# Performance work log

Hardware: AMD Instinct MI355X
Metric: run time of the kernel (lower is better)

The kernel has to match this reference:

```python
import jax, jax.numpy as jnp
import numpy as np

EPS = 1e-5

def _conv(x, w, b, groups=1, pad=0):
    # x: NCHW, w: OIHW (I = in_ch/groups)
    y = jax.lax.conv_general_dilated(
        x, w, window_strides=(1, 1), padding=[(pad, pad), (pad, pad)],
        feature_group_count=groups,
        dimension_numbers=('NCHW', 'OIHW', 'NCHW'))
    return y + b[None, :, None, None]

def _bn(x, g, b, m, v):
    scale = g * jax.lax.rsqrt(v + EPS)
    return x * scale[None, :, None, None] + (b - m * scale)[None, :, None, None]

def _block(x, w_dw, b_dw, w_pw, b_pw, g, b, m, v, groups):
    h = _conv(x, w_dw, b_dw, groups=groups, pad=1)   # 3x3 grouped conv
    h = _conv(h, w_pw, b_pw)                          # 1x1 pointwise 2C->C
    return jax.nn.relu(_bn(h, g, b, m, v))

def setup_inputs() -> dict:
    key = jax.random.key(0)
    ks = jax.random.split(key, 16)
    B, C, H, W = 4, 256, 64, 64
    s = 0.02  # small weight scale to keep softmax logits well-conditioned
    return {
        'x1': jax.random.normal(ks[0], (B, C, H, W), jnp.float32),
        'x2': jax.random.normal(ks[1], (B, C, H, W), jnp.float32),
        'w1_dw': jax.random.normal(ks[2], (2 * C, 2, 3, 3), jnp.float32) * s,
        'b1_dw': jnp.zeros((2 * C,), jnp.float32),
        'w1_pw': jax.random.normal(ks[3], (C, 2 * C, 1, 1), jnp.float32) * s,
        'b1_pw': jnp.zeros((C,), jnp.float32),
        'bn1_g': jnp.ones((C,), jnp.float32),
        'bn1_b': jnp.zeros((C,), jnp.float32),
        'bn1_m': jnp.zeros((C,), jnp.float32),
        'bn1_v': jnp.ones((C,), jnp.float32),
        'w2_dw': jax.random.normal(ks[4], (2 * C, 2, 3, 3), jnp.float32) * s,
        'b2_dw': jnp.zeros((2 * C,), jnp.float32),
        'w2_pw': jax.random.normal(ks[5], (C, 2 * C, 1, 1), jnp.float32) * s,
        'b2_pw': jnp.zeros((C,), jnp.float32),
        'bn2_g': jnp.ones((C,), jnp.float32),
        'bn2_b': jnp.zeros((C,), jnp.float32),
        'bn2_m': jnp.zeros((C,), jnp.float32),
        'bn2_v': jnp.ones((C,), jnp.float32),
        'wq': jax.random.normal(ks[6], (C // 8, C, 1, 1), jnp.float32) * s,
        'bq': jnp.zeros((C // 8,), jnp.float32),
        'wk': jax.random.normal(ks[7], (C // 8, C, 1, 1), jnp.float32) * s,
        'bk': jnp.zeros((C // 8,), jnp.float32),
        'wv': jax.random.normal(ks[8], (C, C, 1, 1), jnp.float32) * s,
        'bv': jnp.zeros((C,), jnp.float32),
        'gamma': jnp.ones((1,), jnp.float32),
    }

def reference(x1, x2,
              w1_dw, b1_dw, w1_pw, b1_pw, bn1_g, bn1_b, bn1_m, bn1_v,
              w2_dw, b2_dw, w2_pw, b2_pw, bn2_g, bn2_b, bn2_m, bn2_v,
              wq, bq, wk, bk, wv, bv, gamma):
    B, C, H, W = x1.shape
    N = H * W
    sub = x1 - x2
    concat1 = jnp.concatenate([sub, x1], axis=1)  # [B,2C,H,W]
    concat2 = jnp.concatenate([sub, x2], axis=1)
    x3 = _block(concat1, w1_dw, b1_dw, w1_pw, b1_pw, bn1_g, bn1_b, bn1_m, bn1_v, groups=C)
    x4 = _block(concat2, w2_dw, b2_dw, w2_pw, b2_pw, bn2_g, bn2_b, bn2_m, bn2_v, groups=C)
    q = _conv(x4, wq, bq).reshape(B, -1, N)   # [B, C//8, N]
    k = _conv(x3, wk, bk).reshape(B, -1, N)   # [B, C//8, N]
    v = _conv(x3, wv, bv).reshape(B, C, N)    # [B, C, N]
    energy = jnp.einsum('bdq,bdk->bqk', q, k)          # [B, N, N]
    attn = jax.nn.softmax(energy, axis=-1)
    out = jnp.einsum('bck,bqk->bcq', v, attn)          # [B, C, N]
    out = out.reshape(B, C, H, W)
    return gamma[0] * out + x1
```

## Files before the change

### kernel.cpp

```cpp
#include <hip/hip_runtime.h>
#include <hip/hip_bf16.h>

#define EPSB 1e-5f

typedef __hip_bfloat16 bf16;
typedef __attribute__((ext_vector_type(8))) short bf16x8;
typedef __attribute__((ext_vector_type(4))) float f32x4;

__device__ __forceinline__ unsigned short f2bu(float x) {
  bf16 h = __float2bfloat16(x);
  return *reinterpret_cast<unsigned short*>(&h);
}
__device__ __forceinline__ unsigned int pk2(float lo, float hi) {
  return ((unsigned int)f2bu(hi) << 16) | (unsigned int)f2bu(lo);
}

__global__ __launch_bounds__(256) void k_dwconv3(
    const float* __restrict__ x1, const float* __restrict__ x2,
    const float* __restrict__ w1, const float* __restrict__ b1,
    const float* __restrict__ w2, const float* __restrict__ b2,
    bf16* __restrict__ h1, bf16* __restrict__ h2) {
  __shared__ float img[2 * 64 * 64];
  int g = blockIdx.x, b = blockIdx.y;
  int t = threadIdx.x;
  int row = t >> 2, x0 = (t & 3) * 16;
  size_t obase = (((size_t)(b * 512 + 2 * g)) << 12) + row * 64 + x0;

  auto stencil = [&](const float* wp, float bs0, float bs1, bf16* hout) {
    float o0[16], o1[16];
#pragma unroll
    for (int i = 0; i < 16; i++) { o0[i] = bs0; o1[i] = bs1; }
#pragma unroll
    for (int ch = 0; ch < 2; ch++) {
      float wa[9], wb[9];
#pragma unroll
      for (int i = 0; i < 9; i++) { wa[i] = wp[ch * 9 + i]; wb[i] = wp[18 + ch * 9 + i]; }
      const float* ib = img + ch * 4096;
#pragma unroll
      for (int ky = 0; ky < 3; ky++) {
        int yy = row + ky - 1;
        if (yy < 0 || yy > 63) continue;
        float v[18];
#pragma unroll
        for (int c = 0; c < 18; c++) {
          int xx = x0 + c - 1;
          v[c] = (xx >= 0 && xx < 64) ? ib[yy * 64 + xx] : 0.f;
        }
        float a0 = wa[ky * 3], a1 = wa[ky * 3 + 1], a2 = wa[ky * 3 + 2];
        float c0 = wb[ky * 3], c1 = wb[ky * 3 + 1], c2 = wb[ky * 3 + 2];
#pragma unroll
        for (int i = 0; i < 16; i++) {
          o0[i] += a0 * v[i] + a1 * v[i + 1] + a2 * v[i + 2];
          o1[i] += c0 * v[i] + c1 * v[i + 1] + c2 * v[i + 2];
        }
      }
    }
    uint4 u0 = {pk2(o0[0], o0[1]), pk2(o0[2], o0[3]), pk2(o0[4], o0[5]), pk2(o0[6], o0[7])};
    uint4 u1 = {pk2(o0[8], o0[9]), pk2(o0[10], o0[11]), pk2(o0[12], o0[13]), pk2(o0[14], o0[15])};
    *(uint4*)&hout[obase] = u0;
    *(uint4*)&hout[obase + 8] = u1;
    uint4 w0 = {pk2(o1[0], o1[1]), pk2(o1[2], o1[3]), pk2(o1[4], o1[5]), pk2(o1[6], o1[7])};
    uint4 w1v = {pk2(o1[8], o1[9]), pk2(o1[10], o1[11]), pk2(o1[12], o1[13]), pk2(o1[14], o1[15])};
    *(uint4*)&hout[obase + 4096] = w0;
    *(uint4*)&hout[obase + 4096 + 8] = w1v;
  };

  if (g < 128) {
    const float4* p1 = (const float4*)(x1 + ((size_t)(b * 256 + 2 * g) << 12));
    const float4* p2 = (const float4*)(x2 + ((size_t)(b * 256 + 2 * g) << 12));
#pragma unroll
    for (int u = 0; u < 8; u++) {
      int i = u * 256 + t;
      float4 a = p1[i], c = p2[i];
      float4 d = {a.x - c.x, a.y - c.y, a.z - c.z, a.w - c.w};
      ((float4*)img)[i] = d;
    }
  } else {
    const float4* p1 = (const float4*)(x1 + ((size_t)(b * 256 + 2 * (g - 128)) << 12));
#pragma unroll
    for (int u = 0; u < 8; u++) {
      int i = u * 256 + t;
      ((float4*)img)[i] = p1[i];
    }
  }
  __syncthreads();
  stencil(w1 + (size_t)(2 * g) * 18, b1[2 * g], b1[2 * g + 1], h1);

  if (g >= 128) {
    __syncthreads();
    const float4* p2 = (const float4*)(x2 + ((size_t)(b * 256 + 2 * (g - 128)) << 12));
#pragma unroll
    for (int u = 0; u < 8; u++) {
      int i = u * 256 + t;
      ((float4*)img)[i] = p2[i];
    }
    __syncthreads();
  }
  stencil(w2 + (size_t)(2 * g) * 18, b2[2 * g], b2[2 * g + 1], h2);
}

__global__ __launch_bounds__(256) void k_gemm_mfma(
    const bf16* __restrict__ In, const float* __restrict__ W,
    const float* __restrict__ bias,
    const float* __restrict__ bng, const float* __restrict__ bnb,
    const float* __restrict__ bnm, const float* __restrict__ bnv,
    int has_bn, int relu,
    bf16* __restrict__ Out, int IC) {
  __shared__ __align__(16) bf16 Al[128][40];
  __shared__ __align__(16) bf16 Bl[64][40];

  int t = threadIdx.x;
  int w = t >> 6, lane = t & 63, l16 = lane & 15, quad = lane >> 4;
  int wr = w >> 1, wc = w & 1;
  int p0 = blockIdx.x * 64;
  int oc0 = blockIdx.y * 128;
  int b = blockIdx.z;
  const bf16* Inb = In + (size_t)b * IC * 4096;

  f32x4 acc[4][2];
#pragma unroll
  for (int mi = 0; mi < 4; mi++)
#pragma unroll
    for (int nj = 0; nj < 2; nj++) acc[mi][nj] = (f32x4){0.f, 0.f, 0.f, 0.f};

  int sl = t & 15, srp = t >> 4;
  int ocl = t >> 1, kb = (t & 1) * 16;

  for (int kc = 0; kc < IC; kc += 32) {
    __syncthreads();
    {
      const float* src = W + (size_t)(oc0 + ocl) * IC + kc + kb;
      float4 f0 = *(const float4*)(src);
      float4 f1 = *(const float4*)(src + 4);
      float4 f2 = *(const float4*)(src + 8);
      float4 f3 = *(const float4*)(src + 12);
      uint4 u0 = {pk2(f0.x, f0.y), pk2(f0.z, f0.w), pk2(f1.x, f1.y), pk2(f1.z, f1.w)};
      uint4 u1 = {pk2(f2.x, f2.y), pk2(f2.z, f2.w), pk2(f3.x, f3.y), pk2(f3.z, f3.w)};
      *(uint4*)&Al[ocl][kb] = u0;
      *(uint4*)&Al[ocl][kb + 8] = u1;
    }
    {
      const unsigned short* re = (const unsigned short*)(Inb + (size_t)(kc + 2 * srp) * 4096 + p0 + sl);
#pragma unroll
      for (int j = 0; j < 4; j++) {
        unsigned int e = re[j * 16];
        unsigned int o = re[4096 + j * 16];
        *(unsigned int*)&Bl[j * 16 + sl][2 * srp] = e | (o << 16);
      }
    }
    __syncthreads();
    bf16x8 af[4], bv[2];
#pragma unroll
    for (int mi = 0; mi < 4; mi++)
      af[mi] = *(const bf16x8*)&Al[wr * 64 + mi * 16 + l16][quad * 8];
#pragma unroll
    for (int nj = 0; nj < 2; nj++)
      bv[nj] = *(const bf16x8*)&Bl[wc * 32 + nj * 16 + l16][quad * 8];
#pragma unroll
    for (int mi = 0; mi < 4; mi++)
#pragma unroll
      for (int nj = 0; nj < 2; nj++)
        acc[mi][nj] = __builtin_amdgcn_mfma_f32_16x16x32_bf16(
            af[mi], bv[nj], acc[mi][nj], 0, 0, 0);
  }

#pragma unroll
  for (int mi = 0; mi < 4; mi++) {
    int ocb = oc0 + wr * 64 + mi * 16 + quad * 4;
    float4 bs4 = *(const float4*)&bias[ocb];
    float4 sc4 = {1.f, 1.f, 1.f, 1.f}, sh4 = bs4;
    if (has_bn) {
      float4 g4 = *(const float4*)&bng[ocb];
      float4 b4 = *(const float4*)&bnb[ocb];
      float4 m4 = *(const float4*)&bnm[ocb];
      float4 v4 = *(const float4*)&bnv[ocb];
      sc4.x = g4.x * rsqrtf(v4.x + EPSB); sh4.x = bs4.x * sc4.x + b4.x - m4.x * sc4.x;
      sc4.y = g4.y * rsqrtf(v4.y + EPSB); sh4.y = bs4.y * sc4.y + b4.y - m4.y * sc4.y;
      sc4.z = g4.z * rsqrtf(v4.z + EPSB); sh4.z = bs4.z * sc4.z + b4.z - m4.z * sc4.z;
      sc4.w = g4.w * rsqrtf(v4.w + EPSB); sh4.w = bs4.w * sc4.w + b4.w - m4.w * sc4.w;
    }
    float sc[4] = {sc4.x, sc4.y, sc4.z, sc4.w};
    float sh[4] = {sh4.x, sh4.y, sh4.z, sh4.w};
#pragma unroll
    for (int nj = 0; nj < 2; nj++) {
      int p = p0 + wc * 32 + nj * 16 + l16;
#pragma unroll
      for (int r = 0; r < 4; r++) {
        float val = acc[mi][nj][r] * sc[r] + sh[r];
        if (relu) val = fmaxf(val, 0.f);
        Out[(((size_t)(b * 256 + ocb + r)) << 12) + p] = __float2bfloat16(val);
      }
    }
  }
}

__global__ __launch_bounds__(256) void k_gemm_qk(
    const bf16* __restrict__ x4, const bf16* __restrict__ x3,
    const float* __restrict__ wq, const float* __restrict__ wk,
    const float* __restrict__ bq, const float* __restrict__ bk,
    bf16* __restrict__ qb, bf16* __restrict__ kb) {
  __shared__ __align__(16) bf16 Al[32][40];
  __shared__ __align__(16) bf16 Bl[128][40];

  int t = threadIdx.x;
  int w = t >> 6, lane = t & 63, l16 = lane & 15, quad = lane >> 4;
  int p0 = blockIdx.x * 128;
  int b = blockIdx.z;
  const bf16* In  = (blockIdx.y == 0) ? x4 : x3;
  const float* W  = (blockIdx.y == 0) ? wq : wk;
  const float* bi = (blockIdx.y == 0) ? bq : bk;
  bf16* Out       = (blockIdx.y == 0) ? qb : kb;
  const bf16* Inb = In + (size_t)b * 256 * 4096;

  f32x4 acc[2][2];
#pragma unroll
  for (int mi = 0; mi < 2; mi++)
#pragma unroll
    for (int nj = 0; nj < 2; nj++) acc[mi][nj] = (f32x4){0.f, 0.f, 0.f, 0.f};

  int aocl = t >> 3, akb = (t & 7) * 4;
  int sl = t & 15, srp = t >> 4;

  for (int kc = 0; kc < 256; kc += 32) {
    __syncthreads();
    {
      const float* src = W + (size_t)aocl * 256 + kc + akb;
      float4 f0 = *(const float4*)(src);
      uint2 u = {pk2(f0.x, f0.y), pk2(f0.z, f0.w)};
      *(uint2*)&Al[aocl][akb] = u;
    }
    {
      const unsigned short* re = (const unsigned short*)(Inb + (size_t)(kc + 2 * srp) * 4096 + p0 + sl);
#pragma unroll
      for (int j = 0; j < 8; j++) {
        unsigned int e = re[j * 16];
        unsigned int o = re[4096 + j * 16];
        *(unsigned int*)&Bl[j * 16 + sl][2 * srp] = e | (o << 16);
      }
    }
    __syncthreads();
    bf16x8 af[2], bv[2];
#pragma unroll
    for (int mi = 0; mi < 2; mi++)
      af[mi] = *(const bf16x8*)&Al[mi * 16 + l16][quad * 8];
#pragma unroll
    for (int nj = 0; nj < 2; nj++)
      bv[nj] = *(const bf16x8*)&Bl[w * 32 + nj * 16 + l16][quad * 8];
#pragma unroll
    for (int mi = 0; mi < 2; mi++)
#pragma unroll
      for (int nj = 0; nj < 2; nj++)
        acc[mi][nj] = __builtin_amdgcn_mfma_f32_16x16x32_bf16(
            af[mi], bv[nj], acc[mi][nj], 0, 0, 0);
  }

#pragma unroll
  for (int mi = 0; mi < 2; mi++) {
    int ocb = mi * 16 + quad * 4;
    float4 bs4 = *(const float4*)&bi[ocb];
    float bs[4] = {bs4.x, bs4.y, bs4.z, bs4.w};
#pragma unroll
    for (int nj = 0; nj < 2; nj++) {
      int p = p0 + w * 32 + nj * 16 + l16;
      float v0 = acc[mi][nj][0] + bs[0];
      float v1 = acc[mi][nj][1] + bs[1];
      float v2 = acc[mi][nj][2] + bs[2];
      float v3 = acc[mi][nj][3] + bs[3];
      uint2 u = {pk2(v0, v1), pk2(v2, v3)};
      *(uint2*)&Out[((size_t)(b * 4096) + p) * 32 + ocb] = u;
    }
  }
}

__global__ __launch_bounds__(512, 4) void k_attn_mfma(
    const bf16* __restrict__ qb, const bf16* __restrict__ kb,
    const bf16* __restrict__ vb, const float* __restrict__ x1,
    const float* __restrict__ gamma, float* __restrict__ out) {
  __shared__ __align__(16) bf16 Pl[2][64 * 128];
  __shared__ float lsumw[8][64];

  int t = threadIdx.x;
  int w = t >> 6, lane = t & 63;
  int l16 = lane & 15, quad = lane >> 4;
  int bx = blockIdx.x;
  int q0 = (bx >> 1) * 64;
  int chalf = bx & 1;
  int b = blockIdx.y;

  const bf16* kbb = kb + (size_t)b * 4096 * 32;
  const bf16* vbb = vb + ((size_t)(b * 256 + chalf * 128)) * 4096;

  bf16x8 qf[4];
#pragma unroll
  for (int nj = 0; nj < 4; nj++)
    qf[nj] = *(const bf16x8*)(qb + ((size_t)(b * 4096 + q0 + nj * 16 + l16)) * 32 + quad * 8);

  f32x4 acc[4];
#pragma unroll
  for (int nj = 0; nj < 4; nj++) acc[nj] = (f32x4){0.f, 0.f, 0.f, 0.f};
  float lpart[4] = {0.f, 0.f, 0.f, 0.f};

  const bf16* kptr = kbb + ((size_t)(w * 16 + l16)) * 32 + quad * 8;
  const bf16* vptr = vbb + ((size_t)(w * 16 + l16)) * 4096 + quad * 8;

  int c16w = w * 2 + (quad >> 1);
  int off8 = (quad & 1) * 4;

  auto load_kv = [&](int j0, bf16x8& kf, bf16x8 vf[4]) {
    kf = *(const bf16x8*)(kptr + (size_t)j0 * 32);
#pragma unroll
    for (int kc = 0; kc < 4; kc++)
      vf[kc] = *(const bf16x8*)(vptr + j0 + kc * 32);
  };

  auto s_phase = [&](const bf16x8& kf, int pb) {
    bf16* P = Pl[pb];
#pragma unroll
    for (int nj = 0; nj < 4; nj++) {
      f32x4 s = __builtin_amdgcn_mfma_f32_16x16x32_bf16(
          kf, qf[nj], (f32x4){0.f, 0.f, 0.f, 0.f}, 0, 0, 0);
      float p0f = __expf(fminf(s[0], 80.f));
      float p1f = __expf(fminf(s[1], 80.f));
      float p2f = __expf(fminf(s[2], 80.f));
      float p3f = __expf(fminf(s[3], 80.f));
      lpart[nj] += (p0f + p1f) + (p2f + p3f);
      int row = nj * 16 + l16;
      int c16 = c16w ^ (row & 15);
      uint2 u = {pk2(p0f, p1f), pk2(p2f, p3f)};
      *(uint2*)&P[row * 128 + c16 * 8 + off8] = u;
    }
  };

  auto pv_phase = [&](const bf16x8 vf[4], int pb) {
    const bf16* P = Pl[pb];
#pragma unroll
    for (int kc = 0; kc < 4; kc++) {
      bf16x8 pf[4];
#pragma unroll
      for (int nj = 0; nj < 4; nj++) {
        int row = nj * 16 + l16;
        int c16 = (kc * 4 + quad) ^ (row & 15);
        pf[nj] = *(const bf16x8*)&P[row * 128 + c16 * 8];
      }
#pragma unroll
      for (int nj = 0; nj < 4; nj++)
        acc[nj] = __builtin_amdgcn_mfma_f32_16x16x32_bf16(
            vf[kc], pf[nj], acc[nj], 0, 0, 0);
    }
  };

  bf16x8 kfA, kfB, vfA[4], vfB[4];
  load_kv(0, kfA, vfA);
  s_phase(kfA, 0);

  for (int i = 0; i < 32; i += 2) {
    __syncthreads();
    if (i < 31) load_kv((i + 1) * 128, kfB, vfB);
    pv_phase(vfA, 0);
    if (i < 31) s_phase(kfB, 1);
    __syncthreads();
    if (i + 2 < 32) load_kv((i + 2) * 128, kfA, vfA);
    if (i + 1 < 32) pv_phase(vfB, 1);
    if (i + 2 < 32) s_phase(kfA, 0);
  }

#pragma unroll
  for (int nj = 0; nj < 4; nj++) {
    float v = lpart[nj];
    v += __shfl_xor(v, 16);
    v += __shfl_xor(v, 32);
    lpart[nj] = v;
  }
  if (lane < 16) {
#pragma unroll
    for (int nj = 0; nj < 4; nj++) lsumw[w][nj * 16 + lane] = lpart[nj];
  }
  __syncthreads();

  float gm = gamma[0];
#pragma unroll
  for (int nj = 0; nj < 4; nj++) {
    int ql = nj * 16 + l16;
    float ls = 0.f;
#pragma unroll
    for (int w8 = 0; w8 < 8; w8++) ls += lsumw[w8][ql];
    float gl = gm / ls;
    int cb = chalf * 128 + w * 16 + quad * 4;
#pragma unroll
    for (int r = 0; r < 4; r++) {
      size_t gidx = (((size_t)(b * 256 + cb + r)) << 12) + q0 + ql;
      out[gidx] = gl * acc[nj][r] + x1[gidx];
    }
  }
}

extern "C" void kernel_launch(void* const* d_in, const int* in_sizes, int n_in,
                              void* d_out, int out_size, void* d_ws, size_t ws_size,
                              hipStream_t stream) {
  const float* x1    = (const float*)d_in[0];
  const float* x2    = (const float*)d_in[1];
  const float* w1_dw = (const float*)d_in[2];
  const float* b1_dw = (const float*)d_in[3];
  const float* w1_pw = (const float*)d_in[4];
  const float* b1_pw = (const float*)d_in[5];
  const float* bn1_g = (const float*)d_in[6];
  const float* bn1_b = (const float*)d_in[7];
  const float* bn1_m = (const float*)d_in[8];
  const float* bn1_v = (const float*)d_in[9];
  const float* w2_dw = (const float*)d_in[10];
  const float* b2_dw = (const float*)d_in[11];
  const float* w2_pw = (const float*)d_in[12];
  const float* b2_pw = (const float*)d_in[13];
  const float* bn2_g = (const float*)d_in[14];
  const float* bn2_b = (const float*)d_in[15];
  const float* bn2_m = (const float*)d_in[16];
  const float* bn2_v = (const float*)d_in[17];
  const float* wq    = (const float*)d_in[18];
  const float* bq    = (const float*)d_in[19];
  const float* wk    = (const float*)d_in[20];
  const float* bk    = (const float*)d_in[21];
  const float* wv    = (const float*)d_in[22];
  const float* bv    = (const float*)d_in[23];
  const float* gamma = (const float*)d_in[24];

  bf16* wsb = (bf16*)d_ws;
  bf16* h1  = wsb;
  bf16* h2  = wsb + 8388608;
  bf16* x3  = wsb + 16777216;
  bf16* x4  = wsb + 20971520;
  bf16* qbf = wsb + 25165824;
  bf16* kbf = wsb + 25690112;
  bf16* vvb = wsb + 26214400;

  k_dwconv3<<<dim3(256, 4), 256, 0, stream>>>(x1, x2, w1_dw, b1_dw, w2_dw, b2_dw, h1, h2);
  k_gemm_mfma<<<dim3(64, 2, 4), 256, 0, stream>>>(h1, w1_pw, b1_pw, bn1_g, bn1_b,
                                                  bn1_m, bn1_v, 1, 1, x3, 512);
  k_gemm_mfma<<<dim3(64, 2, 4), 256, 0, stream>>>(h2, w2_pw, b2_pw, bn2_g, bn2_b,
                                                  bn2_m, bn2_v, 1, 1, x4, 512);

  k_gemm_qk<<<dim3(32, 2, 4), 256, 0, stream>>>(x4, x3, wq, wk, bq, bk, qbf, kbf);
  k_gemm_mfma<<<dim3(64, 2, 4), 256, 0, stream>>>(x3, wv, bv, nullptr, nullptr,
                                                  nullptr, nullptr, 0, 0, vvb, 256);

  k_attn_mfma<<<dim3(128, 4), 512, 0, stream>>>(qbf, kbf, vvb, x1, gamma, (float*)d_out);
}
```

Before: 287.1 us.

## Retile attention to 32 queries x all 256 channels with XCD-aware block mapping

The attention kernel now gives each block 32 queries and all 256 output channels, where it used to take 64 queries and half the channels. This removes the duplicated QK^T/exp work that the two channel-half blocks each did. Block indices are remapped so that blocks sharing a batch land on the same XCD, for better L2 reuse of K/V. The V loads are split from the K loads and issued later, after the P·V phase, which shrinks live registers and changes how load latency overlaps compute. The grid launch must match the new 128-wide linear indexing (the launch code is not shown).

```diff
diff --git a/kernel.cpp b/kernel.cpp
--- a/kernel.cpp
+++ b/kernel.cpp
@@ -276,47 +276,56 @@
     const bf16* __restrict__ qb, const bf16* __restrict__ kb,
     const bf16* __restrict__ vb, const float* __restrict__ x1,
     const float* __restrict__ gamma, float* __restrict__ out) {
-  __shared__ __align__(16) bf16 Pl[2][64 * 128];
-  __shared__ float lsumw[8][64];
+  __shared__ __align__(16) bf16 Pl[2][32 * 128];
+  __shared__ float lsumw[8][32];
 
   int t = threadIdx.x;
   int w = t >> 6, lane = t & 63;
   int l16 = lane & 15, quad = lane >> 4;
-  int bx = blockIdx.x;
-  int q0 = (bx >> 1) * 64;
-  int chalf = bx & 1;
-  int b = blockIdx.y;
+
+  int lin = blockIdx.y * 128 + blockIdx.x;
+  int xcd = lin & 7, slot = lin >> 3;
+  int b = xcd >> 1;
+  int q0 = (slot * 2 + (xcd & 1)) * 32;
 
   const bf16* kbb = kb + (size_t)b * 4096 * 32;
-  const bf16* vbb = vb + ((size_t)(b * 256 + chalf * 128)) * 4096;
-
-  bf16x8 qf[4];
-#pragma unroll
-  for (int nj = 0; nj < 4; nj++)
+  const bf16* vbb = vb + (size_t)b * 256 * 4096;
+
+  bf16x8 qf[2];
+#pragma unroll
+  for (int nj = 0; nj < 2; nj++)
     qf[nj] = *(const bf16x8*)(qb + ((size_t)(b * 4096 + q0 + nj * 16 + l16)) * 32 + quad * 8);
 
-  f32x4 acc[4];
-#pragma unroll
-  for (int nj = 0; nj < 4; nj++) acc[nj] = (f32x4){0.f, 0.f, 0.f, 0.f};
-  float lpart[4] = {0.f, 0.f, 0.f, 0.f};
+  f32x4 acc[2][2];
+#pragma unroll
+  for (int cj = 0; cj < 2; cj++)
+#pragma unroll
+    for (int nj = 0; nj < 2; nj++) acc[cj][nj] = (f32x4){0.f, 0.f, 0.f, 0.f};
+  float lpart[2] = {0.f, 0.f};
 
   const bf16* kptr = kbb + ((size_t)(w * 16 + l16)) * 32 + quad * 8;
-  const bf16* vptr = vbb + ((size_t)(w * 16 + l16)) * 4096 + quad * 8;
+  const bf16* vptr = vbb + ((size_t)(w * 32 + l16)) * 4096 + quad * 8;
 
   int c16w = w * 2 + (quad >> 1);
   int off8 = (quad & 1) * 4;
 
-  auto load_kv = [&](int j0, bf16x8& kf, bf16x8 vf[4]) {
+  bf16x8 kfA, kfB, vf[2][4];
+
+  auto load_k = [&](int j0, bf16x8& kf) {
     kf = *(const bf16x8*)(kptr + (size_t)j0 * 32);
-#pragma unroll
-    for (int kc = 0; kc < 4; kc++)
-      vf[kc] = *(const bf16x8*)(vptr + j0 + kc * 32);
+  };
+  auto load_v = [&](int j0) {
+#pragma unroll
+    for (int cj = 0; cj < 2; cj++)
+#pragma unroll
+      for (int kc = 0; kc < 4; kc++)
+        vf[cj][kc] = *(const bf16x8*)(vptr + (size_t)cj * 16 * 4096 + j0 + kc * 32);
   };
 
   auto s_phase = [&](const bf16x8& kf, int pb) {
     bf16* P = Pl[pb];
 #pragma unroll
-    for (int nj = 0; nj < 4; nj++) {
+    for (int nj = 0; nj < 2; nj++) {
       f32x4 s = __builtin_amdgcn_mfma_f32_16x16x32_bf16(
           kf, qf[nj], (f32x4){0.f, 0.f, 0.f, 0.f}, 0, 0, 0);
       float p0f = __expf(fminf(s[0], 80.f));
@@ -331,41 +340,49 @@
     }
   };
 
-  auto pv_phase = [&](const bf16x8 vf[4], int pb) {
+  auto pv_phase = [&](int pb) {
     const bf16* P = Pl[pb];
 #pragma unroll
     for (int kc = 0; kc < 4; kc++) {
-      bf16x8 pf[4];
-#pragma unroll
-      for (int nj = 0; nj < 4; nj++) {
+      bf16x8 pf[2];
+#pragma unroll
+      for (int nj = 0; nj < 2; nj++) {
         int row = nj * 16 + l16;
         int c16 = (kc * 4 + quad) ^ (row & 15);
         pf[nj] = *(const bf16x8*)&P[row * 128 + c16 * 8];
       }
 #pragma unroll
-      for (int nj = 0; nj < 4; nj++)
-        acc[nj] = __builtin_amdgcn_mfma_f32_16x16x32_bf16(
-            vf[kc], pf[nj], acc[nj], 0, 0, 0);
+      for (int nj = 0; nj < 2; nj++)
+#pragma unroll
+        for (int cj = 0; cj < 2; cj++)
+          acc[cj][nj] = __builtin_amdgcn_mfma_f32_16x16x32_bf16(
+              vf[cj][kc], pf[nj], acc[cj][nj], 0, 0, 0);
     }
   };
 
-  bf16x8 kfA, kfB, vfA[4], vfB[4];
-  load_kv(0, kfA, vfA);
+  load_k(0, kfA);
+  load_v(0);
   s_phase(kfA, 0);
 
   for (int i = 0; i < 32; i += 2) {
-    __syncthreads();
-    if (i < 31) load_kv((i + 1) * 128, kfB, vfB);
-    pv_phase(vfA, 0);
-    if (i < 31) s_phase(kfB, 1);
-    __syncthreads();
-    if (i + 2 < 32) load_kv((i + 2) * 128, kfA, vfA);
-    if (i + 1 < 32) pv_phase(vfB, 1);
-    if (i + 2 < 32) s_phase(kfA, 0);
-  }
-
-#pragma unroll
-  for (int nj = 0; nj < 4; nj++) {
+    if (i + 1 < 32) load_k((i + 1) * 128, kfB);
+    __syncthreads();
+    pv_phase(0);
+    if (i + 1 < 32) {
+      load_v((i + 1) * 128);
+      s_phase(kfB, 1);
+    }
+    if (i + 2 < 32) load_k((i + 2) * 128, kfA);
+    __syncthreads();
+    pv_phase(1);
+    if (i + 2 < 32) {
+      load_v((i + 2) * 128);
+      s_phase(kfA, 0);
+    }
+  }
+
+#pragma unroll
+  for (int nj = 0; nj < 2; nj++) {
     float v = lpart[nj];
     v += __shfl_xor(v, 16);
     v += __shfl_xor(v, 32);
@@ -373,23 +390,26 @@
   }
   if (lane < 16) {
 #pragma unroll
-    for (int nj = 0; nj < 4; nj++) lsumw[w][nj * 16 + lane] = lpart[nj];
+    for (int nj = 0; nj < 2; nj++) lsumw[w][nj * 16 + lane] = lpart[nj];
   }
   __syncthreads();
 
   float gm = gamma[0];
 #pragma unroll
-  for (int nj = 0; nj < 4; nj++) {
+  for (int nj = 0; nj < 2; nj++) {
     int ql = nj * 16 + l16;
     float ls = 0.f;
 #pragma unroll
     for (int w8 = 0; w8 < 8; w8++) ls += lsumw[w8][ql];
     float gl = gm / ls;
-    int cb = chalf * 128 + w * 16 + quad * 4;
-#pragma unroll
-    for (int r = 0; r < 4; r++) {
-      size_t gidx = (((size_t)(b * 256 + cb + r)) << 12) + q0 + ql;
-      out[gidx] = gl * acc[nj][r] + x1[gidx];
+#pragma unroll
+    for (int cj = 0; cj < 2; cj++) {
+      int cb = w * 32 + cj * 16 + quad * 4;
+#pragma unroll
+      for (int r = 0; r < 4; r++) {
+        size_t gidx = (((size_t)(b * 256 + cb + r)) << 12) + q0 + ql;
+        out[gidx] = gl * acc[cj][nj][r] + x1[gidx];
+      }
     }
   }
 }
```

New measurement: 331.6 us. 1.16x slower.
